# Kernel tuning notes

Hardware: AMD Instinct MI355X
Metric: run time of the kernel (lower is better)

Reference implementation:

```python
import jax, jax.numpy as jnp
import numpy as np

K = 4          # Chebyshev order
N = 8192       # nodes
I = 128        # input_size
H = 256        # hidden_size
E = 262144     # nnz in Laplacian


def _uniform(key, shape, bound):
    return jax.random.uniform(key, shape, jnp.float32, -bound, bound)


def setup_inputs() -> dict:
    key = jax.random.key(0)
    ks = jax.random.split(key, 20)
    bound = np.sqrt(1.0 / I)
    inp = {
        "x": jax.random.normal(ks[0], (N, I), jnp.float32),
        "h": jax.random.normal(ks[1], (N, H), jnp.float32),
        "c": jax.random.normal(ks[2], (N, H), jnp.float32),
        "lap_vals": 0.1 * jax.random.normal(ks[3], (E,), jnp.float32),
        "pos": jax.random.randint(ks[4], (E, 2), 0, N, jnp.int64),
        "W_fh": _uniform(ks[5], (K, H, H), bound),
        "W_fx": _uniform(ks[6], (K, H, I), bound),
        "bf": _uniform(ks[7], (N, H), bound),
        "W_ih": _uniform(ks[8], (K, H, H), bound),
        "W_ix": _uniform(ks[9], (K, H, I), bound),
        "bi": _uniform(ks[10], (N, H), bound),
        "W_oh": _uniform(ks[11], (K, H, H), bound),
        "W_ox": _uniform(ks[12], (K, H, I), bound),
        "bo": _uniform(ks[13], (N, H), bound),
        "W_ch": _uniform(ks[14], (K, H, H), bound),
        "W_cx": _uniform(ks[15], (K, H, I), bound),
        "bc": _uniform(ks[16], (N, H), bound),
    }
    return inp


def cheb_features(L, X):
    # T_k(L) @ X via the 3-term recurrence applied to vectors (no N x N powers).
    Ts = [X, L @ X]
    for _ in range(2, K):
        Ts.append(2.0 * (L @ Ts[-1]) - Ts[-2])
    return jnp.stack(Ts[:K])  # [K, N, F]


def graph_conv(TX, W):
    # sum_k T_k(L) X W_k^T ; TX: [K,N,F], W: [K,H,F] -> [N,H]
    return jnp.einsum("knf,khf->nh", TX, W)


def reference(x, h, c, lap_vals, pos, W_fh, W_fx, bf, W_ih, W_ix, bi,
              W_oh, W_ox, bo, W_ch, W_cx, bc):
    L = jnp.zeros((N, N), jnp.float32).at[pos[:, 0], pos[:, 1]].set(lap_vals)
    Th = cheb_features(L, h)  # [K,N,H]
    Tx = cheb_features(L, x)  # [K,N,I]
    f = jax.nn.sigmoid(graph_conv(Th, W_fh) + graph_conv(Tx, W_fx) + bf)
    i = jax.nn.sigmoid(graph_conv(Th, W_ih) + graph_conv(Tx, W_ix) + bi)
    o = jax.nn.sigmoid(graph_conv(Th, W_oh) + graph_conv(Tx, W_ox) + bo)
    c_new = i * jnp.tanh(graph_conv(Th, W_ch) + graph_conv(Tx, W_cx) + bc) + f * c
    h_new = o * jnp.tanh(c_new)
    return (h_new, c_new)
```

## Files before the change

### kernel.cpp

```cpp
#include <hip/hip_runtime.h>
#include <hip/hip_bf16.h>
#include <cstdint>

#define NN 8192
#define HH 256
#define II 128
#define KORD 4
#define EE 262144
#define KW 1536
#define MW 1024
#define RCAP 128
#define BK 64

typedef __attribute__((ext_vector_type(8))) short bf16x8;
typedef __attribute__((ext_vector_type(8))) unsigned short u16x8;
typedef __attribute__((ext_vector_type(4))) float f32x4;

__device__ __forceinline__ float bf2f(unsigned short u) {
    union { uint32_t i; float f; } x; x.i = ((uint32_t)u) << 16; return x.f;
}
__device__ __forceinline__ unsigned short f2bf(float f) {
    __hip_bfloat16 b = __float2bfloat16(f);
    return *(unsigned short*)&b;
}

__device__ __forceinline__ void read_pos(const int* __restrict__ pos, int flag,
                                         int e, int& r, int& c) {
    if (flag) { r = pos[4 * e]; c = pos[4 * e + 2]; }
    else      { r = pos[2 * e]; c = pos[2 * e + 1]; }
}

__global__ void init_small(uint32_t* __restrict__ rcnt,
                           const int* __restrict__ pos, int* __restrict__ flag) {
    int i = blockIdx.x * blockDim.x + threadIdx.x;
    if (i < NN) rcnt[i] = 0u;
    if (i == 0) {
        int f = 1;
        for (int k = 0; k < 128; ++k) {
            if (pos[2 * k + 1] != 0) { f = 0; break; }
        }
        *flag = f;
    }
}

__global__ void scatter_fixed(const int* __restrict__ pos, const int* __restrict__ flagp,
                              const float* __restrict__ lap,
                              uint32_t* __restrict__ rcnt, uint2* __restrict__ cpack) {
    int e = blockIdx.x * blockDim.x + threadIdx.x;
    if (e >= EE) return;
    int flag = *flagp;
    int r, c; read_pos(pos, flag, e, r, c);
    uint32_t slot = atomicAdd(&rcnt[r], 1u);
    if (slot < RCAP) {
        uint2 p;
        p.x = ((uint32_t)(e + 1) << 13) | (uint32_t)c;
        p.y = __float_as_uint(lap[e]);
        cpack[(size_t)r * RCAP + slot] = p;
    }
}

__global__ __launch_bounds__(256) void dedup_rows(uint32_t* __restrict__ rcnt,
                                                  uint2* __restrict__ cpack) {
    int r = blockIdx.x * 4 + (threadIdx.x >> 6);
    int lane = threadIdx.x & 63;
    uint32_t lenu = rcnt[r];
    int len = (lenu > RCAP) ? RCAP : (int)lenu;
    uint2* base = &cpack[(size_t)r * RCAP];
    uint32_t m0 = 0u, m1 = 0u;
    if (lane < len) m0 = base[lane].x;
    if (64 + lane < len) m1 = base[64 + lane].x;
    bool lose0 = false, lose1 = false;
    int nchunk = (len + 63) >> 6;
    for (int ch = 0; ch < nchunk; ++ch) {
        int cl = len - ch * 64; if (cl > 64) cl = 64;
        for (int i = 0; i < cl; ++i) {
            uint32_t mi = __shfl(ch == 0 ? m0 : m1, i);
            lose0 |= (((mi ^ m0) & 8191u) == 0u) && (mi > m0);
            lose1 |= (((mi ^ m1) & 8191u) == 0u) && (mi > m1);
        }
    }
    if (lane < len) {
        base[lane].x = m0 & 8191u;
        if (lose0) base[lane].y = 0u;
    }
    if (64 + lane < len) {
        base[64 + lane].x = m1 & 8191u;
        if (lose1) base[64 + lane].y = 0u;
    }
    if (lane == 0 && lenu > RCAP) rcnt[r] = RCAP;
}

template <int F, bool LAST>
__device__ __forceinline__ void spmv_seg(
    const uint32_t* __restrict__ rcnt, const uint2* __restrict__ cp,
    const unsigned short* __restrict__ Xb, const unsigned short* __restrict__ Pb,
    unsigned short* __restrict__ Yb, unsigned short* __restrict__ Am, int colbase,
    float a, float b, int r, int lane) {
    uint32_t len = rcnt[r]; if (len > RCAP) len = RCAP;
    uint32_t s = (uint32_t)r * RCAP, e = s + len;
    int off = lane * 8;
    float acc[8];
#pragma unroll
    for (int j = 0; j < 8; ++j) acc[j] = 0.0f;
    uint32_t i = s;
    for (; i + 4 <= e; i += 4) {
        uint2 p0 = cp[i], p1 = cp[i + 1], p2 = cp[i + 2], p3 = cp[i + 3];
        u16x8 g0 = *(const u16x8*)&Xb[(size_t)p0.x * F + off];
        u16x8 g1 = *(const u16x8*)&Xb[(size_t)p1.x * F + off];
        u16x8 g2 = *(const u16x8*)&Xb[(size_t)p2.x * F + off];
        u16x8 g3 = *(const u16x8*)&Xb[(size_t)p3.x * F + off];
        float v0 = __uint_as_float(p0.y), v1 = __uint_as_float(p1.y);
        float v2 = __uint_as_float(p2.y), v3 = __uint_as_float(p3.y);
#pragma unroll
        for (int j = 0; j < 8; ++j)
            acc[j] += v0 * bf2f(g0[j]) + v1 * bf2f(g1[j]) +
                      v2 * bf2f(g2[j]) + v3 * bf2f(g3[j]);
    }
    for (; i < e; ++i) {
        uint2 p0 = cp[i];
        u16x8 g0 = *(const u16x8*)&Xb[(size_t)p0.x * F + off];
        float v0 = __uint_as_float(p0.y);
#pragma unroll
        for (int j = 0; j < 8; ++j) acc[j] += v0 * bf2f(g0[j]);
    }
    u16x8 ob;
    if (b != 0.0f) {
        u16x8 pv = *(const u16x8*)&Pb[(size_t)r * F + off];
#pragma unroll
        for (int j = 0; j < 8; ++j) ob[j] = f2bf(a * acc[j] + b * bf2f(pv[j]));
    } else {
#pragma unroll
        for (int j = 0; j < 8; ++j) ob[j] = f2bf(a * acc[j]);
    }
    if (!LAST) *(u16x8*)&Yb[(size_t)r * F + off] = ob;
    *(u16x8*)&Am[(size_t)r * KW + colbase + off] = ob;
}

#define NBH (NN / 8)
#define NBX (NN / 16)
template <bool LAST>
__global__ __launch_bounds__(256) void spmv_cheb_dual(
    const uint32_t* __restrict__ rcnt, const uint2* __restrict__ cp,
    const unsigned short* __restrict__ Xh, const unsigned short* __restrict__ Ph,
    unsigned short* __restrict__ Yh, int cbh,
    const unsigned short* __restrict__ Xx, const unsigned short* __restrict__ Px,
    unsigned short* __restrict__ Yx, int cbx,
    unsigned short* __restrict__ Am, float a, float b) {
    int bid = blockIdx.x, t = threadIdx.x;
    if (bid < NBH) {
        int r = bid * 8 + (t >> 5), lane = t & 31;
        spmv_seg<HH, LAST>(rcnt, cp, Xh, Ph, Yh, Am, cbh, a, b, r, lane);
    } else {
        int r = (bid - NBH) * 16 + (t >> 4), lane = t & 15;
        spmv_seg<II, LAST>(rcnt, cp, Xx, Px, Yx, Am, cbx, a, b, r, lane);
    }
}

__global__ void pack_T0(const float* __restrict__ h, const float* __restrict__ x,
                        unsigned short* __restrict__ Hb, unsigned short* __restrict__ Xb,
                        unsigned short* __restrict__ Am) {
    int idx = blockIdx.x * blockDim.x + threadIdx.x;
    if (idx >= NN * 96) return;
    int n, q, col;
    const float* src;
    unsigned short* st;
    if (idx < NN * 64) { n = idx >> 6; q = (idx & 63) * 4; src = &h[(size_t)n * HH + q]; st = &Hb[(size_t)n * HH + q]; col = q; }
    else { int ix = idx - NN * 64; n = ix >> 5; q = (ix & 31) * 4; src = &x[(size_t)n * II + q]; st = &Xb[(size_t)n * II + q]; col = 1024 + q; }
    float4 v = *(const float4*)src;
    ushort4 pk;
    pk.x = f2bf(v.x); pk.y = f2bf(v.y); pk.z = f2bf(v.z); pk.w = f2bf(v.w);
    *(ushort4*)st = pk;
    *(ushort4*)&Am[(size_t)n * KW + col] = pk;
}

__global__ void pack_B(const float* __restrict__ Wfh, const float* __restrict__ Wih,
                       const float* __restrict__ Woh, const float* __restrict__ Wch,
                       const float* __restrict__ Wfx, const float* __restrict__ Wix,
                       const float* __restrict__ Wox, const float* __restrict__ Wcx,
                       __hip_bfloat16* __restrict__ Bm) {
    int idx = blockIdx.x * blockDim.x + threadIdx.x;
    if (idx >= MW * KW) return;
    int m = idx / KW, j = idx - m * KW;
    int g = m >> 8, hh = m & 255;
    const float* Wh = (g == 0) ? Wfh : (g == 1) ? Wih : (g == 2) ? Woh : Wch;
    const float* Wx = (g == 0) ? Wfx : (g == 1) ? Wix : (g == 2) ? Wox : Wcx;
    float v;
    if (j < 1024) { int k = j >> 8, f = j & 255; v = Wh[((size_t)k * HH + hh) * HH + f]; }
    else { int jj = j - 1024; int k = jj >> 7, f = jj & 127; v = Wx[((size_t)k * HH + hh) * II + f]; }
    Bm[idx] = __float2bfloat16(v);
}

__device__ __forceinline__ void gload_lds16(const void* g, void* l) {
    __builtin_amdgcn_global_load_lds(
        (const __attribute__((address_space(1))) void*)g,
        (__attribute__((address_space(3))) void*)l, 16, 0, 0);
}

__device__ __forceinline__ void stage_side(const __hip_bfloat16* __restrict__ G,
                                           int r0, int kk, int t, short* lds) {
#pragma unroll
    for (int s = 0; s < 4; ++s) {
        int e = (s * 256 + t) * 8;
        int row = e >> 6;
        int kks = ((((e >> 3) & 7) ^ (row & 7)) << 3);
        gload_lds16(&G[(size_t)(r0 + row) * KW + kk + kks], &lds[e]);
    }
}

__global__ __launch_bounds__(256) void gemm_mfma(
    const __hip_bfloat16* __restrict__ A,
    const __hip_bfloat16* __restrict__ B,
    float* __restrict__ C) {
    __shared__ short Alds[2][128 * BK];
    __shared__ short Blds[2][128 * BK];
    int bid = blockIdx.x;
    int sw = (bid & 7) * 64 + (bid >> 3);
    int m0 = (sw & 7) * 128;
    int n0 = (sw >> 3) * 128;
    int t = threadIdx.x;
    int w = t >> 6, l = t & 63;
    int wr = w >> 1, wc = w & 1;
    int lrow = l & 15, q = l >> 4;

    f32x4 acc[4][4];
#pragma unroll
    for (int i = 0; i < 4; ++i)
#pragma unroll
        for (int j = 0; j < 4; ++j) acc[i][j] = (f32x4)0.0f;

    stage_side(A, n0, 0, t, Alds[0]);
    stage_side(B, m0, 0, t, Blds[0]);
    __syncthreads();

    int cur = 0;
    for (int k0 = 0; k0 < KW; k0 += BK) {
        if (k0 + BK < KW) {
            stage_side(A, n0, k0 + BK, t, Alds[cur ^ 1]);
            stage_side(B, m0, k0 + BK, t, Blds[cur ^ 1]);
        }
#pragma unroll
        for (int h = 0; h < 2; ++h) {
            int sl = (((h << 2) | q) ^ (lrow & 7)) << 3;
            bf16x8 af[4], bfr[4];
#pragma unroll
            for (int i = 0; i < 4; ++i)
                af[i] = *(const bf16x8*)&Alds[cur][(wr * 64 + i * 16 + lrow) * BK + sl];
#pragma unroll
            for (int j = 0; j < 4; ++j)
                bfr[j] = *(const bf16x8*)&Blds[cur][(wc * 64 + j * 16 + lrow) * BK + sl];
#pragma unroll
            for (int i = 0; i < 4; ++i)
#pragma unroll
                for (int j = 0; j < 4; ++j)
                    acc[i][j] = __builtin_amdgcn_mfma_f32_16x16x32_bf16(af[i], bfr[j], acc[i][j], 0, 0, 0);
        }
        __syncthreads();
        cur ^= 1;
    }

    int r4 = (l >> 4) * 4;
#pragma unroll
    for (int i = 0; i < 4; ++i)
#pragma unroll
        for (int j = 0; j < 4; ++j)
#pragma unroll
            for (int r = 0; r < 4; ++r) {
                int row = n0 + wr * 64 + i * 16 + r4 + r;
                int col = m0 + wc * 64 + j * 16 + lrow;
                C[(size_t)row * MW + col] = acc[i][j][r];
            }
}

__device__ __forceinline__ float sigmoidf_(float x) { return 1.0f / (1.0f + expf(-x)); }

__global__ __launch_bounds__(256) void lstm_ew(
    const float* __restrict__ C,
    const float* __restrict__ bf, const float* __restrict__ bi,
    const float* __restrict__ bo, const float* __restrict__ bc,
    const float* __restrict__ cin, float* __restrict__ out) {
    int i = blockIdx.x * blockDim.x + threadIdx.x;
    if (i >= NN * HH / 4) return;
    int n = i >> 6;
    int h4 = (i & 63) * 4;
    size_t cb = (size_t)n * MW;
    size_t hb = (size_t)n * HH + h4;
    float4 pf = *(const float4*)&C[cb + 0 * HH + h4];
    float4 pi = *(const float4*)&C[cb + 1 * HH + h4];
    float4 po = *(const float4*)&C[cb + 2 * HH + h4];
    float4 pc = *(const float4*)&C[cb + 3 * HH + h4];
    float4 vbf = *(const float4*)&bf[hb];
    float4 vbi = *(const float4*)&bi[hb];
    float4 vbo = *(const float4*)&bo[hb];
    float4 vbc = *(const float4*)&bc[hb];
    float4 vc  = *(const float4*)&cin[hb];
    float4 hn, cn;
    {
        float fg = sigmoidf_(pf.x + vbf.x), ig = sigmoidf_(pi.x + vbi.x);
        float og = sigmoidf_(po.x + vbo.x), cg = tanhf(pc.x + vbc.x);
        cn.x = ig * cg + fg * vc.x; hn.x = og * tanhf(cn.x);
    }
    {
        float fg = sigmoidf_(pf.y + vbf.y), ig = sigmoidf_(pi.y + vbi.y);
        float og = sigmoidf_(po.y + vbo.y), cg = tanhf(pc.y + vbc.y);
        cn.y = ig * cg + fg * vc.y; hn.y = og * tanhf(cn.y);
    }
    {
        float fg = sigmoidf_(pf.z + vbf.z), ig = sigmoidf_(pi.z + vbi.z);
        float og = sigmoidf_(po.z + vbo.z), cg = tanhf(pc.z + vbc.z);
        cn.z = ig * cg + fg * vc.z; hn.z = og * tanhf(cn.z);
    }
    {
        float fg = sigmoidf_(pf.w + vbf.w), ig = sigmoidf_(pi.w + vbi.w);
        float og = sigmoidf_(po.w + vbo.w), cg = tanhf(pc.w + vbc.w);
        cn.w = ig * cg + fg * vc.w; hn.w = og * tanhf(cn.w);
    }
    *(float4*)&out[hb] = hn;
    *(float4*)&out[(size_t)NN * HH + hb] = cn;
}

extern "C" void kernel_launch(void* const* d_in, const int* in_sizes, int n_in,
                              void* d_out, int out_size, void* d_ws, size_t ws_size,
                              hipStream_t stream) {
    const float* x   = (const float*)d_in[0];
    const float* h   = (const float*)d_in[1];
    const float* c   = (const float*)d_in[2];
    const float* lap = (const float*)d_in[3];
    const int*   pos = (const int*)d_in[4];
    const float* Wfh = (const float*)d_in[5];
    const float* Wfx = (const float*)d_in[6];
    const float* bf  = (const float*)d_in[7];
    const float* Wih = (const float*)d_in[8];
    const float* Wix = (const float*)d_in[9];
    const float* bi  = (const float*)d_in[10];
    const float* Woh = (const float*)d_in[11];
    const float* Wox = (const float*)d_in[12];
    const float* bo  = (const float*)d_in[13];
    const float* Wch = (const float*)d_in[14];
    const float* Wcx = (const float*)d_in[15];
    const float* bc  = (const float*)d_in[16];
    float* out = (float*)d_out;

    uint8_t* ws = (uint8_t*)d_ws;
    size_t off = 0;
    auto take = [&](size_t bytes) -> void* {
        void* p = ws + off;
        off += (bytes + 255) & ~(size_t)255;
        return p;
    };
    int*      flag = (int*)take(4);
    uint32_t* rcnt = (uint32_t*)take((size_t)NN * 4);
    uint2*    cpack= (uint2*)take((size_t)NN * RCAP * 8);
    unsigned short* Hb = (unsigned short*)take((size_t)3 * NN * HH * 2);
    unsigned short* Xb = (unsigned short*)take((size_t)3 * NN * II * 2);
    unsigned short* Amat = (unsigned short*)take((size_t)NN * KW * 2);
    __hip_bfloat16* Bmat = (__hip_bfloat16*)take((size_t)MW * KW * 2);
    float*    Cpre = (float*)take((size_t)NN * MW * 4);

    init_small<<<NN / 256, 256, 0, stream>>>(rcnt, pos, flag);
    scatter_fixed<<<EE / 256, 256, 0, stream>>>(pos, flag, lap, rcnt, cpack);
    dedup_rows<<<NN / 4, 256, 0, stream>>>(rcnt, cpack);

    pack_T0<<<(NN * 96 + 255) / 256, 256, 0, stream>>>(h, x, Hb, Xb, Amat);
    pack_B<<<(MW * KW + 255) / 256, 256, 0, stream>>>(Wfh, Wih, Woh, Wch,
                                                      Wfx, Wix, Wox, Wcx, Bmat);

    unsigned short* Hb0 = Hb;
    unsigned short* Hb1 = Hb + (size_t)NN * HH;
    unsigned short* Hb2 = Hb1 + (size_t)NN * HH;
    unsigned short* Xb0 = Xb;
    unsigned short* Xb1 = Xb + (size_t)NN * II;
    unsigned short* Xb2 = Xb1 + (size_t)NN * II;

    int sg = NBH + NBX;
    spmv_cheb_dual<false><<<sg, 256, 0, stream>>>(rcnt, cpack,
        Hb0, Hb0, Hb1, 256, Xb0, Xb0, Xb1, 1152, Amat, 1.0f, 0.0f);
    spmv_cheb_dual<false><<<sg, 256, 0, stream>>>(rcnt, cpack,
        Hb1, Hb0, Hb2, 512, Xb1, Xb0, Xb2, 1280, Amat, 2.0f, -1.0f);
    spmv_cheb_dual<true><<<sg, 256, 0, stream>>>(rcnt, cpack,
        Hb2, Hb1, nullptr, 768, Xb2, Xb1, nullptr, 1408, Amat, 2.0f, -1.0f);

    gemm_mfma<<<512, 256, 0, stream>>>((const __hip_bfloat16*)Amat, Bmat, Cpre);

    lstm_ew<<<(NN * HH / 4 + 255) / 256, 256, 0, stream>>>(Cpre, bf, bi, bo, bc, c, out);
}
```

Measured before the change: 162.8 us.

## Compact sparse entries to 32-bit and gather SpMV directly from GEMM A-matrix

Dedup now writes a compact 4-byte entry per nonzero (bf16 value in the high half, column in the low half) into a new array, halving index/value traffic in each SpMV pass. The separate Hb/Xb Chebyshev buffers are removed: SpMV reads its source and previous terms from, and writes its output to, column slices of the GEMM A matrix, so duplicate stores go away. The cost is that Laplacian values are rounded to bf16, and gathers now use a 3 KB row stride, which may give worse cache locality than the packed 512/256-byte rows.

```diff
diff --git a/kernel.cpp b/kernel.cpp
--- a/kernel.cpp
+++ b/kernel.cpp
@@ -60,15 +60,17 @@
 }
 
 __global__ __launch_bounds__(256) void dedup_rows(uint32_t* __restrict__ rcnt,
-                                                  uint2* __restrict__ cpack) {
+                                                  const uint2* __restrict__ cpack,
+                                                  uint32_t* __restrict__ cpk) {
     int r = blockIdx.x * 4 + (threadIdx.x >> 6);
     int lane = threadIdx.x & 63;
     uint32_t lenu = rcnt[r];
     int len = (lenu > RCAP) ? RCAP : (int)lenu;
-    uint2* base = &cpack[(size_t)r * RCAP];
+    const uint2* base = &cpack[(size_t)r * RCAP];
     uint32_t m0 = 0u, m1 = 0u;
-    if (lane < len) m0 = base[lane].x;
-    if (64 + lane < len) m1 = base[64 + lane].x;
+    float v0 = 0.0f, v1 = 0.0f;
+    if (lane < len) { uint2 p = base[lane]; m0 = p.x; v0 = __uint_as_float(p.y); }
+    if (64 + lane < len) { uint2 p = base[64 + lane]; m1 = p.x; v1 = __uint_as_float(p.y); }
     bool lose0 = false, lose1 = false;
     int nchunk = (len + 63) >> 6;
     for (int ch = 0; ch < nchunk; ++ch) {
@@ -79,22 +81,18 @@
             lose1 |= (((mi ^ m1) & 8191u) == 0u) && (mi > m1);
         }
     }
-    if (lane < len) {
-        base[lane].x = m0 & 8191u;
-        if (lose0) base[lane].y = 0u;
-    }
-    if (64 + lane < len) {
-        base[64 + lane].x = m1 & 8191u;
-        if (lose1) base[64 + lane].y = 0u;
-    }
+    uint32_t* ob = &cpk[(size_t)r * RCAP];
+    if (lane < len)
+        ob[lane] = ((uint32_t)f2bf(lose0 ? 0.0f : v0) << 16) | (m0 & 8191u);
+    if (64 + lane < len)
+        ob[64 + lane] = ((uint32_t)f2bf(lose1 ? 0.0f : v1) << 16) | (m1 & 8191u);
     if (lane == 0 && lenu > RCAP) rcnt[r] = RCAP;
 }
 
-template <int F, bool LAST>
+template <int F>
 __device__ __forceinline__ void spmv_seg(
-    const uint32_t* __restrict__ rcnt, const uint2* __restrict__ cp,
-    const unsigned short* __restrict__ Xb, const unsigned short* __restrict__ Pb,
-    unsigned short* __restrict__ Yb, unsigned short* __restrict__ Am, int colbase,
+    const uint32_t* __restrict__ rcnt, const uint32_t* __restrict__ cpk,
+    unsigned short* Am, int cbsrc, int cbprev, int cbdst,
     float a, float b, int r, int lane) {
     uint32_t len = rcnt[r]; if (len > RCAP) len = RCAP;
     uint32_t s = (uint32_t)r * RCAP, e = s + len;
@@ -104,72 +102,68 @@
     for (int j = 0; j < 8; ++j) acc[j] = 0.0f;
     uint32_t i = s;
     for (; i + 4 <= e; i += 4) {
-        uint2 p0 = cp[i], p1 = cp[i + 1], p2 = cp[i + 2], p3 = cp[i + 3];
-        u16x8 g0 = *(const u16x8*)&Xb[(size_t)p0.x * F + off];
-        u16x8 g1 = *(const u16x8*)&Xb[(size_t)p1.x * F + off];
-        u16x8 g2 = *(const u16x8*)&Xb[(size_t)p2.x * F + off];
-        u16x8 g3 = *(const u16x8*)&Xb[(size_t)p3.x * F + off];
-        float v0 = __uint_as_float(p0.y), v1 = __uint_as_float(p1.y);
-        float v2 = __uint_as_float(p2.y), v3 = __uint_as_float(p3.y);
+        uint32_t p0 = cpk[i], p1 = cpk[i + 1], p2 = cpk[i + 2], p3 = cpk[i + 3];
+        u16x8 g0 = *(const u16x8*)&Am[(size_t)(p0 & 8191u) * KW + cbsrc + off];
+        u16x8 g1 = *(const u16x8*)&Am[(size_t)(p1 & 8191u) * KW + cbsrc + off];
+        u16x8 g2 = *(const u16x8*)&Am[(size_t)(p2 & 8191u) * KW + cbsrc + off];
+        u16x8 g3 = *(const u16x8*)&Am[(size_t)(p3 & 8191u) * KW + cbsrc + off];
+        float v0 = bf2f((unsigned short)(p0 >> 16));
+        float v1 = bf2f((unsigned short)(p1 >> 16));
+        float v2 = bf2f((unsigned short)(p2 >> 16));
+        float v3 = bf2f((unsigned short)(p3 >> 16));
 #pragma unroll
         for (int j = 0; j < 8; ++j)
             acc[j] += v0 * bf2f(g0[j]) + v1 * bf2f(g1[j]) +
                       v2 * bf2f(g2[j]) + v3 * bf2f(g3[j]);
     }
     for (; i < e; ++i) {
-        uint2 p0 = cp[i];
-        u16x8 g0 = *(const u16x8*)&Xb[(size_t)p0.x * F + off];
-        float v0 = __uint_as_float(p0.y);
+        uint32_t p0 = cpk[i];
+        u16x8 g0 = *(const u16x8*)&Am[(size_t)(p0 & 8191u) * KW + cbsrc + off];
+        float v0 = bf2f((unsigned short)(p0 >> 16));
 #pragma unroll
         for (int j = 0; j < 8; ++j) acc[j] += v0 * bf2f(g0[j]);
     }
     u16x8 ob;
     if (b != 0.0f) {
-        u16x8 pv = *(const u16x8*)&Pb[(size_t)r * F + off];
+        u16x8 pv = *(const u16x8*)&Am[(size_t)r * KW + cbprev + off];
 #pragma unroll
         for (int j = 0; j < 8; ++j) ob[j] = f2bf(a * acc[j] + b * bf2f(pv[j]));
     } else {
 #pragma unroll
         for (int j = 0; j < 8; ++j) ob[j] = f2bf(a * acc[j]);
     }
-    if (!LAST) *(u16x8*)&Yb[(size_t)r * F + off] = ob;
-    *(u16x8*)&Am[(size_t)r * KW + colbase + off] = ob;
+    *(u16x8*)&Am[(size_t)r * KW + cbdst + off] = ob;
 }
 
 #define NBH (NN / 8)
 #define NBX (NN / 16)
-template <bool LAST>
 __global__ __launch_bounds__(256) void spmv_cheb_dual(
-    const uint32_t* __restrict__ rcnt, const uint2* __restrict__ cp,
-    const unsigned short* __restrict__ Xh, const unsigned short* __restrict__ Ph,
-    unsigned short* __restrict__ Yh, int cbh,
-    const unsigned short* __restrict__ Xx, const unsigned short* __restrict__ Px,
-    unsigned short* __restrict__ Yx, int cbx,
-    unsigned short* __restrict__ Am, float a, float b) {
+    const uint32_t* __restrict__ rcnt, const uint32_t* __restrict__ cpk,
+    unsigned short* Am,
+    int sh, int ph, int dh,
+    int sx, int px, int dx,
+    float a, float b) {
     int bid = blockIdx.x, t = threadIdx.x;
     if (bid < NBH) {
         int r = bid * 8 + (t >> 5), lane = t & 31;
-        spmv_seg<HH, LAST>(rcnt, cp, Xh, Ph, Yh, Am, cbh, a, b, r, lane);
+        spmv_seg<HH>(rcnt, cpk, Am, sh, ph, dh, a, b, r, lane);
     } else {
         int r = (bid - NBH) * 16 + (t >> 4), lane = t & 15;
-        spmv_seg<II, LAST>(rcnt, cp, Xx, Px, Yx, Am, cbx, a, b, r, lane);
+        spmv_seg<II>(rcnt, cpk, Am, sx, px, dx, a, b, r, lane);
     }
 }
 
 __global__ void pack_T0(const float* __restrict__ h, const float* __restrict__ x,
-                        unsigned short* __restrict__ Hb, unsigned short* __restrict__ Xb,
                         unsigned short* __restrict__ Am) {
     int idx = blockIdx.x * blockDim.x + threadIdx.x;
     if (idx >= NN * 96) return;
     int n, q, col;
     const float* src;
-    unsigned short* st;
-    if (idx < NN * 64) { n = idx >> 6; q = (idx & 63) * 4; src = &h[(size_t)n * HH + q]; st = &Hb[(size_t)n * HH + q]; col = q; }
-    else { int ix = idx - NN * 64; n = ix >> 5; q = (ix & 31) * 4; src = &x[(size_t)n * II + q]; st = &Xb[(size_t)n * II + q]; col = 1024 + q; }
+    if (idx < NN * 64) { n = idx >> 6; q = (idx & 63) * 4; src = &h[(size_t)n * HH + q]; col = q; }
+    else { int ix = idx - NN * 64; n = ix >> 5; q = (ix & 31) * 4; src = &x[(size_t)n * II + q]; col = 1024 + q; }
     float4 v = *(const float4*)src;
     ushort4 pk;
     pk.x = f2bf(v.x); pk.y = f2bf(v.y); pk.z = f2bf(v.z); pk.w = f2bf(v.w);
-    *(ushort4*)st = pk;
     *(ushort4*)&Am[(size_t)n * KW + col] = pk;
 }
 
@@ -350,34 +344,26 @@
     int*      flag = (int*)take(4);
     uint32_t* rcnt = (uint32_t*)take((size_t)NN * 4);
     uint2*    cpack= (uint2*)take((size_t)NN * RCAP * 8);
-    unsigned short* Hb = (unsigned short*)take((size_t)3 * NN * HH * 2);
-    unsigned short* Xb = (unsigned short*)take((size_t)3 * NN * II * 2);
+    uint32_t* cpk  = (uint32_t*)take((size_t)NN * RCAP * 4);
     unsigned short* Amat = (unsigned short*)take((size_t)NN * KW * 2);
     __hip_bfloat16* Bmat = (__hip_bfloat16*)take((size_t)MW * KW * 2);
     float*    Cpre = (float*)take((size_t)NN * MW * 4);
 
     init_small<<<NN / 256, 256, 0, stream>>>(rcnt, pos, flag);
     scatter_fixed<<<EE / 256, 256, 0, stream>>>(pos, flag, lap, rcnt, cpack);
-    dedup_rows<<<NN / 4, 256, 0, stream>>>(rcnt, cpack);
-
-    pack_T0<<<(NN * 96 + 255) / 256, 256, 0, stream>>>(h, x, Hb, Xb, Amat);
+    dedup_rows<<<NN / 4, 256, 0, stream>>>(rcnt, cpack, cpk);
+
+    pack_T0<<<(NN * 96 + 255) / 256, 256, 0, stream>>>(h, x, Amat);
     pack_B<<<(MW * KW + 255) / 256, 256, 0, stream>>>(Wfh, Wih, Woh, Wch,
                                                       Wfx, Wix, Wox, Wcx, Bmat);
 
-    unsigned short* Hb0 = Hb;
-    unsigned short* Hb1 = Hb + (size_t)NN * HH;
-    unsigned short* Hb2 = Hb1 + (size_t)NN * HH;
-    unsigned short* Xb0 = Xb;
-    unsigned short* Xb1 = Xb + (size_t)NN * II;
-    unsigned short* Xb2 = Xb1 + (size_t)NN * II;
-
     int sg = NBH + NBX;
-    spmv_cheb_dual<false><<<sg, 256, 0, stream>>>(rcnt, cpack,
-        Hb0, Hb0, Hb1, 256, Xb0, Xb0, Xb1, 1152, Amat, 1.0f, 0.0f);
-    spmv_cheb_dual<false><<<sg, 256, 0, stream>>>(rcnt, cpack,
-        Hb1, Hb0, Hb2, 512, Xb1, Xb0, Xb2, 1280, Amat, 2.0f, -1.0f);
-    spmv_cheb_dual<true><<<sg, 256, 0, stream>>>(rcnt, cpack,
-        Hb2, Hb1, nullptr, 768, Xb2, Xb1, nullptr, 1408, Amat, 2.0f, -1.0f);
+    spmv_cheb_dual<<<sg, 256, 0, stream>>>(rcnt, cpk, Amat,
+        0, 0, 256, 1024, 1024, 1152, 1.0f, 0.0f);
+    spmv_cheb_dual<<<sg, 256, 0, stream>>>(rcnt, cpk, Amat,
+        256, 0, 512, 1152, 1024, 1280, 2.0f, -1.0f);
+    spmv_cheb_dual<<<sg, 256, 0, stream>>>(rcnt, cpk, Amat,
+        512, 256, 768, 1280, 1152, 1408, 2.0f, -1.0f);
 
     gemm_mfma<<<512, 256, 0, stream>>>((const __hip_bfloat16*)Amat, Bmat, Cpre);
 
```

Result: no change. 164.1 us (+0.8%).
